# Performance work log

Measured on AMD Instinct MI355X. Metric: run time of the kernel, lower is better.

## Reference

```python
import jax, jax.numpy as jnp
import numpy as np

B, C, N = 8, 3, 4096
NSAMPLE = 10
MLP = (64, 64)
# checkerboard re-gather pattern from the original module
INDS = np.array([0, 1, 2, 3, 2, 3, 4, 5, 4, 5, 6, 7, 6, 7, 8, 9])


def setup_inputs() -> dict:
    key = jax.random.key(0)
    k1, k2, k3 = jax.random.split(key, 3)
    pos = jax.random.normal(k1, (B, C, N), jnp.float32)
    w1 = jax.random.normal(k2, (MLP[0], 4 * C, 2, 2), jnp.float32) * 0.1  # Conv2d(12, mlp0, k=2)
    b1 = jnp.zeros((MLP[0],), jnp.float32)
    w2 = jax.random.normal(k3, (MLP[1], MLP[0]), jnp.float32) * 0.1       # Conv2d(mlp0, mlp1, k=1)
    b2 = jnp.zeros((MLP[1],), jnp.float32)
    return {"pos": pos, "w1": w1, "b1": b1, "w2": w2, "b2": b2}


def _squeeze_2x2_alt(x):
    # x: [B, N, c, 4, 4] -> [B, N, 4c, 2, 2] with channel order [a, d, b, c]
    a = x[..., 0::2, 0::2]  # (0,0) of each 2x2 block
    d = x[..., 1::2, 1::2]  # (1,1)
    b = x[..., 0::2, 1::2]  # (0,1)
    c = x[..., 1::2, 0::2]  # (1,0)
    return jnp.concatenate([a, d, b, c], axis=-3)


def reference(pos, w1, b1, w2, b2):
    Bn, Cn, Nn = pos.shape
    pos_t = pos.transpose(0, 2, 1)  # [B, N, C]
    # pairwise squared distances [B, N, N]
    sq = jnp.sum(pos_t * pos_t, axis=-1)
    d2 = sq[:, :, None] - 2.0 * jnp.einsum('bnc,bmc->bnm', pos_t, pos_t) + sq[:, None, :]
    _, idx = jax.lax.top_k(-d2, NSAMPLE)  # [B, N, K] nearest neighbors (self first)
    # grouping_operation: grouped[b,c,n,k] = pos[b,c,idx[b,n,k]]
    grouped = jax.vmap(lambda p, i: p[:, i])(pos, idx)  # [B, C, N, K]
    pg = grouped[..., INDS]                              # [B, C, N, 16]
    pg = pg.transpose(0, 2, 1, 3).reshape(Bn, Nn, Cn, 4, 4)  # [B, N, 3, 4, 4]
    sqz = _squeeze_2x2_alt(pg)                           # [B, N, 12, 2, 2]
    # Conv2d(12->mlp0, k=2, stride=1) over 2x2 spatial == full contraction
    h = jnp.einsum('bnchw,ochw->bno', sqz, w1) + b1      # [B, N, mlp0]
    out = jnp.einsum('bno,po->bnp', h, w2) + b2          # [B, N, mlp1]
    return out.transpose(0, 2, 1)                        # [B, mlp1, N]
```

## Files before the change

kernel.cpp:

```cpp
#include <hip/hip_runtime.h>
#include <math.h>

#define NPTS 4096
#define NSMP 10

typedef float f32x2 __attribute__((ext_vector_type(2)));

__global__ __launch_bounds__(256) void prep_kernel(
    const float* __restrict__ w1, const float* __restrict__ b1,
    const float* __restrict__ w2, const float* __restrict__ b2,
    float* __restrict__ wn, float* __restrict__ bb) {
  __shared__ float w1l[64 * 48];
  __shared__ float w2t[64 * 64];
  __shared__ float b1l[64];
  __shared__ float part[4][30][64];
  __shared__ float bpart[4][64];
  const int t = threadIdx.x, p = t & 63, grp = t >> 6, o0 = grp * 16;
  for (int idx = t; idx < 64 * 48; idx += 256) w1l[idx] = w1[idx];
  for (int idx = t; idx < 64 * 64; idx += 256) w2t[(idx & 63) * 64 + (idx >> 6)] = w2[idx];
  if (t < 64) b1l[t] = b1[t];
  __syncthreads();

  const int sg[16] = {0,2,4,6, 3,5,7,9, 1,3,5,7, 2,4,6,8};
  float w2r[16];
  #pragma unroll
  for (int oo = 0; oo < 16; ++oo) w2r[oo] = w2t[(o0 + oo) * 64 + p];
  float wloc[30];
  #pragma unroll
  for (int i = 0; i < 30; ++i) wloc[i] = 0.0f;
  #pragma unroll
  for (int g = 0; g < 4; ++g)
    #pragma unroll
    for (int i = 0; i < 2; ++i)
      #pragma unroll
      for (int j = 0; j < 2; ++j) {
        const int s = sg[g * 4 + i * 2 + j];
        #pragma unroll
        for (int c = 0; c < 3; ++c) {
          const int k = (c + 3 * g) * 4 + i * 2 + j;
          float wk = 0.0f;
          #pragma unroll
          for (int oo = 0; oo < 16; ++oo)
            wk = fmaf(w2r[oo], w1l[(o0 + oo) * 48 + k], wk);
          wloc[s * 3 + c] += wk;
        }
      }
  #pragma unroll
  for (int i = 0; i < 30; ++i) part[grp][i][p] = wloc[i];
  float sb = 0.0f;
  #pragma unroll
  for (int oo = 0; oo < 16; ++oo) sb = fmaf(w2r[oo], b1l[o0 + oo], sb);
  bpart[grp][p] = sb;
  __syncthreads();
  const float* p0 = &part[0][0][0];
  for (int idx = t; idx < 30 * 64; idx += 256)
    wn[idx] = p0[idx] + p0[1920 + idx] + p0[3840 + idx] + p0[5760 + idx];
  if (t < 64) bb[t] = b2[t] + bpart[0][t] + bpart[1][t] + bpart[2][t] + bpart[3][t];
}

__global__ __launch_bounds__(1024, 4) void topk_kernel(const float* __restrict__ pos,
                                                       const float* __restrict__ wng,
                                                       const float* __restrict__ bbg,
                                                       float* __restrict__ out) {
  __shared__ float4 pts[NPTS];
  __shared__ int cnt[16][8];
  __shared__ int bufi[16][8][64];
  __shared__ int nbrL[16][8][NSMP];

  const int b = blockIdx.y, tid = threadIdx.x, lane = tid & 63, wv = tid >> 6;
  const float* pb = pos + (size_t)b * 3 * NPTS;
  for (int i = tid; i < NPTS; i += 1024) {
    float x = pb[i], y = pb[i + NPTS], z = pb[i + 2 * NPTS];
    float sq = __fadd_rn(__fadd_rn(__fmul_rn(x, x), __fmul_rn(y, y)), __fmul_rn(z, z));
    pts[i] = make_float4(x, y, z, sq);
  }
  float wnr[30];
  #pragma unroll
  for (int sc = 0; sc < 30; ++sc) wnr[sc] = wng[sc * 64 + lane];
  const float blv = bbg[lane];
  __syncthreads();

  const int n0 = blockIdx.x * 128 + wv * 8;

  f32x2 qx2[4], qy2[4], qz2[4], dmin[4];
  #pragma unroll
  for (int pp = 0; pp < 4; ++pp) {
    float4 qa = pts[n0 + 2 * pp], qb = pts[n0 + 2 * pp + 1];
    qx2[pp].x = -2.0f * qa.x; qx2[pp].y = -2.0f * qb.x;
    qy2[pp].x = -2.0f * qa.y; qy2[pp].y = -2.0f * qb.y;
    qz2[pp].x = -2.0f * qa.z; qz2[pp].y = -2.0f * qb.z;
    dmin[pp].x = INFINITY; dmin[pp].y = INFINITY;
  }

  #pragma unroll 8
  for (int k = 0; k < 64; ++k) {
    float4 p = pts[k * 64 + lane];
    #pragma unroll
    for (int pp = 0; pp < 4; ++pp) {
      f32x2 key = qx2[pp] * p.x + p.w;
      key = qy2[pp] * p.y + key;
      key = qz2[pp] * p.z + key;
      dmin[pp] = __builtin_elementwise_min(dmin[pp], key);
    }
  }

  unsigned um[8], lo[8], hi[8];
  #pragma unroll
  for (int r = 0; r < 8; ++r) {
    float dm = (r & 1) ? dmin[r >> 1].y : dmin[r >> 1].x;
    unsigned ub = __float_as_uint(dm);
    um[r] = (ub & 0x80000000u) ? ~ub : (ub | 0x80000000u);
    lo[r] = 0u; hi[r] = 0xFFFFFFFFu;
  }
  #pragma unroll 1
  for (int it = 0; it < 20; ++it) {
    #pragma unroll
    for (int r = 0; r < 8; ++r) {
      unsigned mid = lo[r] + ((hi[r] - lo[r]) >> 1);
      int c10 = __popcll(__ballot(um[r] <= mid));
      if (c10 >= NSMP) hi[r] = mid; else lo[r] = mid + 1;
    }
  }
  float tx[8];
  #pragma unroll
  for (int r = 0; r < 8; ++r) {
    unsigned tb = (hi[r] & 0x80000000u) ? (hi[r] ^ 0x80000000u) : ~hi[r];
    float tf = __uint_as_float(tb);
    tx[r] = __fadd_rn(__fadd_rn(tf, 2e-4f), __fmul_rn(fabsf(tf), 1e-5f));
  }

  if (lane < 8) cnt[wv][lane] = 0;

  #pragma unroll 4
  for (int k = 0; k < 64; ++k) {
    float4 p = pts[k * 64 + lane];
    #pragma unroll
    for (int pp = 0; pp < 4; ++pp) {
      f32x2 key = qx2[pp] * p.x + p.w;
      key = qy2[pp] * p.y + key;
      key = qz2[pp] * p.z + key;
      if (key.x <= tx[2 * pp]) {
        int ps = atomicAdd(&cnt[wv][2 * pp], 1);
        if (ps < 64) bufi[wv][2 * pp][ps] = k * 64 + lane;
      }
      if (key.y <= tx[2 * pp + 1]) {
        int ps = atomicAdd(&cnt[wv][2 * pp + 1], 1);
        if (ps < 64) bufi[wv][2 * pp + 1][ps] = k * 64 + lane;
      }
    }
  }

  int c[8], si[8], rank[8];
  double dd[8];
  int cmax = 0;
  #pragma unroll
  for (int r = 0; r < 8; ++r) {
    c[r] = __builtin_amdgcn_readfirstlane(cnt[wv][r]);
    if (c[r] > 64) c[r] = 64;
    cmax = (c[r] > cmax) ? c[r] : cmax;
    rank[r] = 0;
  }
  #pragma unroll
  for (int r = 0; r < 8; ++r) {
    float4 qa = pts[n0 + r];
    if (lane < c[r]) {
      si[r] = bufi[wv][r][lane];
      float4 p = pts[si[r]];
      double dqx = (double)qa.x, dqy = (double)qa.y, dqz = (double)qa.z;
      double px = (double)p.x, py = (double)p.y, pz = (double)p.z;
      double dot = dqx * px + dqy * py + dqz * pz;
      double sqn = dqx * dqx + dqy * dqy + dqz * dqz;
      double sqm = px * px + py * py + pz * pz;
      dd[r] = (sqn - 2.0 * dot) + sqm;
    } else { dd[r] = (double)INFINITY; si[r] = 0x7FFFFFFF; }
  }
  #pragma unroll 1
  for (int j = 0; j < cmax; ++j) {
    #pragma unroll
    for (int r = 0; r < 8; ++r) {
      int jlo = __builtin_amdgcn_readlane(__double2loint(dd[r]), j);
      int jhi = __builtin_amdgcn_readlane(__double2hiint(dd[r]), j);
      int ji  = __builtin_amdgcn_readlane(si[r], j);
      double jd = __hiloint2double(jhi, jlo);
      if (jd < dd[r] || (jd == dd[r] && ji < si[r])) ++rank[r];
    }
  }
  #pragma unroll
  for (int r = 0; r < 8; ++r)
    if (lane < c[r] && rank[r] < NSMP)
      nbrL[wv][r][rank[r]] = si[r];

  float acc[8];
  #pragma unroll
  for (int r = 0; r < 8; ++r) acc[r] = blv;
  #pragma unroll 1
  for (int r = 0; r < 8; ++r) {
    float a = acc[r];
    #pragma unroll
    for (int s = 0; s < NSMP; ++s) {
      int id = nbrL[wv][r][s];
      float4 pv = pts[id];
      a = fmaf(wnr[s * 3 + 0], pv.x, a);
      a = fmaf(wnr[s * 3 + 1], pv.y, a);
      a = fmaf(wnr[s * 3 + 2], pv.z, a);
    }
    acc[r] = a;
  }
  float* ob = out + ((size_t)b * 64 + lane) * NPTS + n0;
  float4 v0 = make_float4(acc[0], acc[1], acc[2], acc[3]);
  float4 v1 = make_float4(acc[4], acc[5], acc[6], acc[7]);
  *(float4*)(ob)     = v0;
  *(float4*)(ob + 4) = v1;
}

extern "C" void kernel_launch(void* const* d_in, const int* in_sizes, int n_in,
                              void* d_out, int out_size, void* d_ws, size_t ws_size,
                              hipStream_t stream) {
  (void)in_sizes; (void)n_in; (void)out_size; (void)ws_size;
  const float* pos = (const float*)d_in[0];
  const float* w1  = (const float*)d_in[1];
  const float* b1  = (const float*)d_in[2];
  const float* w2  = (const float*)d_in[3];
  const float* b2  = (const float*)d_in[4];
  float* out = (float*)d_out;

  float* wn = (float*)d_ws;
  float* bb = (float*)((char*)d_ws + 30 * 64 * 4);

  prep_kernel<<<dim3(1), dim3(256), 0, stream>>>(w1, b1, w2, b2, wn, bb);
  topk_kernel<<<dim3(32, 8), dim3(1024), 0, stream>>>(pos, wn, bb, out);
}
```

Before: 135.7 us.

## Fuse weight folding into top-k kernel, radix-select threshold, coalesced LDS-staged output

Removes the separate single-block prep kernel and instead has every block fold w2·w1 (and the bias) into shared memory after staging a transposed w2, which saves one launch and its serialization. The binary-search threshold is replaced with a bitwise radix prefix search that runs 24 ballot rounds instead of 20 with simpler arithmetic. Output is staged through shared memory, reusing the candidate buffer region, and written as coalesced float4 rows instead of strided per-lane 8-float stores. Each of the 256 blocks now redundantly recomputes the folded weights and reads them from LDS in the final MLP step instead of registers. The squared norm also changes to fma form.

```diff
diff --git a/kernel.cpp b/kernel.cpp
--- a/kernel.cpp
+++ b/kernel.cpp
@@ -6,81 +6,65 @@
 
 typedef float f32x2 __attribute__((ext_vector_type(2)));
 
-__global__ __launch_bounds__(256) void prep_kernel(
-    const float* __restrict__ w1, const float* __restrict__ b1,
-    const float* __restrict__ w2, const float* __restrict__ b2,
-    float* __restrict__ wn, float* __restrict__ bb) {
-  __shared__ float w1l[64 * 48];
-  __shared__ float w2t[64 * 64];
-  __shared__ float b1l[64];
-  __shared__ float part[4][30][64];
-  __shared__ float bpart[4][64];
-  const int t = threadIdx.x, p = t & 63, grp = t >> 6, o0 = grp * 16;
-  for (int idx = t; idx < 64 * 48; idx += 256) w1l[idx] = w1[idx];
-  for (int idx = t; idx < 64 * 64; idx += 256) w2t[(idx & 63) * 64 + (idx >> 6)] = w2[idx];
-  if (t < 64) b1l[t] = b1[t];
-  __syncthreads();
-
-  const int sg[16] = {0,2,4,6, 3,5,7,9, 1,3,5,7, 2,4,6,8};
-  float w2r[16];
-  #pragma unroll
-  for (int oo = 0; oo < 16; ++oo) w2r[oo] = w2t[(o0 + oo) * 64 + p];
-  float wloc[30];
-  #pragma unroll
-  for (int i = 0; i < 30; ++i) wloc[i] = 0.0f;
-  #pragma unroll
-  for (int g = 0; g < 4; ++g)
-    #pragma unroll
-    for (int i = 0; i < 2; ++i)
-      #pragma unroll
-      for (int j = 0; j < 2; ++j) {
-        const int s = sg[g * 4 + i * 2 + j];
-        #pragma unroll
-        for (int c = 0; c < 3; ++c) {
-          const int k = (c + 3 * g) * 4 + i * 2 + j;
-          float wk = 0.0f;
-          #pragma unroll
-          for (int oo = 0; oo < 16; ++oo)
-            wk = fmaf(w2r[oo], w1l[(o0 + oo) * 48 + k], wk);
-          wloc[s * 3 + c] += wk;
-        }
-      }
-  #pragma unroll
-  for (int i = 0; i < 30; ++i) part[grp][i][p] = wloc[i];
-  float sb = 0.0f;
-  #pragma unroll
-  for (int oo = 0; oo < 16; ++oo) sb = fmaf(w2r[oo], b1l[o0 + oo], sb);
-  bpart[grp][p] = sb;
-  __syncthreads();
-  const float* p0 = &part[0][0][0];
-  for (int idx = t; idx < 30 * 64; idx += 256)
-    wn[idx] = p0[idx] + p0[1920 + idx] + p0[3840 + idx] + p0[5760 + idx];
-  if (t < 64) bb[t] = b2[t] + bpart[0][t] + bpart[1][t] + bpart[2][t] + bpart[3][t];
-}
-
 __global__ __launch_bounds__(1024, 4) void topk_kernel(const float* __restrict__ pos,
-                                                       const float* __restrict__ wng,
-                                                       const float* __restrict__ bbg,
+                                                       const float* __restrict__ w1,
+                                                       const float* __restrict__ b1,
+                                                       const float* __restrict__ w2,
+                                                       const float* __restrict__ b2,
                                                        float* __restrict__ out) {
   __shared__ float4 pts[NPTS];
-  __shared__ int cnt[16][8];
-  __shared__ int bufi[16][8][64];
-  __shared__ int nbrL[16][8][NSMP];
+  __shared__ float  trans[16 * 520];
+  __shared__ float  wl[30 * 64];
+  __shared__ float  bl[64];
+  __shared__ int    nbrL[16][8][NSMP];
+  __shared__ int    cnt[16][8];
 
   const int b = blockIdx.y, tid = threadIdx.x, lane = tid & 63, wv = tid >> 6;
   const float* pb = pos + (size_t)b * 3 * NPTS;
   for (int i = tid; i < NPTS; i += 1024) {
     float x = pb[i], y = pb[i + NPTS], z = pb[i + 2 * NPTS];
-    float sq = __fadd_rn(__fadd_rn(__fmul_rn(x, x), __fmul_rn(y, y)), __fmul_rn(z, z));
+    float sq = fmaf(z, z, fmaf(y, y, x * x));
     pts[i] = make_float4(x, y, z, sq);
   }
-  float wnr[30];
-  #pragma unroll
-  for (int sc = 0; sc < 30; ++sc) wnr[sc] = wng[sc * 64 + lane];
-  const float blv = bbg[lane];
+  for (int idx = tid; idx < 4096; idx += 1024)
+    trans[(idx & 63) * 65 + (idx >> 6)] = w2[idx];
   __syncthreads();
 
-  const int n0 = blockIdx.x * 128 + wv * 8;
+  {
+    const int occN[10] = {1,1,2,2,2,2,2,2,1,1};
+    const int occG[10][2] = {{0,0},{2,0},{0,3},{1,2},{0,3},{1,2},{0,3},{1,2},{3,0},{1,0}};
+    const int occQ[10][2] = {{0,0},{0,0},{1,0},{0,1},{2,1},{1,2},{3,2},{2,3},{3,0},{3,0}};
+    if (wv < 15) {
+      #pragma unroll
+      for (int slot = 0; slot < 2; ++slot) {
+        int sc = wv + 15 * slot;
+        int s = sc / 3, cc = sc - 3 * s;
+        int k1 = __builtin_amdgcn_readfirstlane((cc + 3 * occG[s][0]) * 4 + occQ[s][0]);
+        int k2 = __builtin_amdgcn_readfirstlane((cc + 3 * occG[s][1]) * 4 + occQ[s][1]);
+        int two = __builtin_amdgcn_readfirstlane(occN[s] - 1);
+        float acc = 0.0f;
+        #pragma unroll 8
+        for (int o = 0; o < 64; ++o) {
+          float wsum = w1[o * 48 + k1];
+          if (two) wsum += w1[o * 48 + k2];
+          acc = fmaf(trans[o * 65 + lane], wsum, acc);
+        }
+        wl[sc * 64 + lane] = acc;
+      }
+    } else {
+      float acc = b2[lane];
+      #pragma unroll 8
+      for (int o = 0; o < 64; ++o)
+        acc = fmaf(trans[o * 65 + lane], b1[o], acc);
+      bl[lane] = acc;
+    }
+  }
+  __syncthreads();
+
+  const int nb = blockIdx.x * 128;
+  const int n0 = nb + wv * 8;
+  float* transF = &trans[wv * 520];
+  int*   bufiW  = (int*)transF;
 
   f32x2 qx2[4], qy2[4], qz2[4], dmin[4];
   #pragma unroll
@@ -104,27 +88,26 @@
     }
   }
 
-  unsigned um[8], lo[8], hi[8];
+  unsigned um[8];
   #pragma unroll
   for (int r = 0; r < 8; ++r) {
     float dm = (r & 1) ? dmin[r >> 1].y : dmin[r >> 1].x;
     unsigned ub = __float_as_uint(dm);
     um[r] = (ub & 0x80000000u) ? ~ub : (ub | 0x80000000u);
-    lo[r] = 0u; hi[r] = 0xFFFFFFFFu;
-  }
+  }
+  unsigned pfx[8] = {0u,0u,0u,0u,0u,0u,0u,0u};
   #pragma unroll 1
-  for (int it = 0; it < 20; ++it) {
-    #pragma unroll
-    for (int r = 0; r < 8; ++r) {
-      unsigned mid = lo[r] + ((hi[r] - lo[r]) >> 1);
-      int c10 = __popcll(__ballot(um[r] <= mid));
-      if (c10 >= NSMP) hi[r] = mid; else lo[r] = mid + 1;
-    }
+  for (int bno = 31; bno >= 8; --bno) {
+    const unsigned bit = 1u << bno, ones = bit - 1u;
+    #pragma unroll
+    for (int r = 0; r < 8; ++r)
+      if (__popcll(__ballot(um[r] <= (pfx[r] | ones))) < NSMP) pfx[r] |= bit;
   }
   float tx[8];
   #pragma unroll
   for (int r = 0; r < 8; ++r) {
-    unsigned tb = (hi[r] & 0x80000000u) ? (hi[r] ^ 0x80000000u) : ~hi[r];
+    unsigned T = pfx[r] | 0xFFu;
+    unsigned tb = (T & 0x80000000u) ? (T ^ 0x80000000u) : ~T;
     float tf = __uint_as_float(tb);
     tx[r] = __fadd_rn(__fadd_rn(tf, 2e-4f), __fmul_rn(fabsf(tf), 1e-5f));
   }
@@ -141,11 +124,11 @@
       key = qz2[pp] * p.z + key;
       if (key.x <= tx[2 * pp]) {
         int ps = atomicAdd(&cnt[wv][2 * pp], 1);
-        if (ps < 64) bufi[wv][2 * pp][ps] = k * 64 + lane;
+        if (ps < 64) bufiW[(2 * pp) * 64 + ps] = k * 64 + lane;
       }
       if (key.y <= tx[2 * pp + 1]) {
         int ps = atomicAdd(&cnt[wv][2 * pp + 1], 1);
-        if (ps < 64) bufi[wv][2 * pp + 1][ps] = k * 64 + lane;
+        if (ps < 64) bufiW[(2 * pp + 1) * 64 + ps] = k * 64 + lane;
       }
     }
   }
@@ -164,13 +147,13 @@
   for (int r = 0; r < 8; ++r) {
     float4 qa = pts[n0 + r];
     if (lane < c[r]) {
-      si[r] = bufi[wv][r][lane];
+      si[r] = bufiW[r * 64 + lane];
       float4 p = pts[si[r]];
       double dqx = (double)qa.x, dqy = (double)qa.y, dqz = (double)qa.z;
-      double px = (double)p.x, py = (double)p.y, pz = (double)p.z;
-      double dot = dqx * px + dqy * py + dqz * pz;
+      double dpx = (double)p.x, dpy = (double)p.y, dpz = (double)p.z;
+      double dot = dqx * dpx + dqy * dpy + dqz * dpz;
       double sqn = dqx * dqx + dqy * dqy + dqz * dqz;
-      double sqm = px * px + py * py + pz * pz;
+      double sqm = dpx * dpx + dpy * dpy + dpz * dpz;
       dd[r] = (sqn - 2.0 * dot) + sqm;
     } else { dd[r] = (double)INFINITY; si[r] = 0x7FFFFFFF; }
   }
@@ -190,33 +173,35 @@
     if (lane < c[r] && rank[r] < NSMP)
       nbrL[wv][r][rank[r]] = si[r];
 
-  float acc[8];
-  #pragma unroll
-  for (int r = 0; r < 8; ++r) acc[r] = blv;
   #pragma unroll 1
   for (int r = 0; r < 8; ++r) {
-    float a = acc[r];
+    float a = bl[lane];
     #pragma unroll
     for (int s = 0; s < NSMP; ++s) {
       int id = nbrL[wv][r][s];
       float4 pv = pts[id];
-      a = fmaf(wnr[s * 3 + 0], pv.x, a);
-      a = fmaf(wnr[s * 3 + 1], pv.y, a);
-      a = fmaf(wnr[s * 3 + 2], pv.z, a);
-    }
-    acc[r] = a;
-  }
-  float* ob = out + ((size_t)b * 64 + lane) * NPTS + n0;
-  float4 v0 = make_float4(acc[0], acc[1], acc[2], acc[3]);
-  float4 v1 = make_float4(acc[4], acc[5], acc[6], acc[7]);
-  *(float4*)(ob)     = v0;
-  *(float4*)(ob + 4) = v1;
+      a = fmaf(wl[(s * 3 + 0) * 64 + lane], pv.x, a);
+      a = fmaf(wl[(s * 3 + 1) * 64 + lane], pv.y, a);
+      a = fmaf(wl[(s * 3 + 2) * 64 + lane], pv.z, a);
+    }
+    transF[r * 65 + lane] = a;
+  }
+  __syncthreads();
+
+  #pragma unroll
+  for (int it = 0; it < 2; ++it) {
+    int p = (tid >> 5) + 32 * it, t32 = tid & 31;
+    const float* src = &trans[(t32 >> 1) * 520 + (t32 & 1) * 4 * 65 + p];
+    float4 v;
+    v.x = src[0 * 65]; v.y = src[1 * 65]; v.z = src[2 * 65]; v.w = src[3 * 65];
+    *(float4*)(out + ((size_t)b * 64 + p) * NPTS + nb + 4 * t32) = v;
+  }
 }
 
 extern "C" void kernel_launch(void* const* d_in, const int* in_sizes, int n_in,
                               void* d_out, int out_size, void* d_ws, size_t ws_size,
                               hipStream_t stream) {
-  (void)in_sizes; (void)n_in; (void)out_size; (void)ws_size;
+  (void)in_sizes; (void)n_in; (void)out_size; (void)d_ws; (void)ws_size;
   const float* pos = (const float*)d_in[0];
   const float* w1  = (const float*)d_in[1];
   const float* b1  = (const float*)d_in[2];
@@ -224,9 +209,5 @@
   const float* b2  = (const float*)d_in[4];
   float* out = (float*)d_out;
 
-  float* wn = (float*)d_ws;
-  float* bb = (float*)((char*)d_ws + 30 * 64 * 4);
-
-  prep_kernel<<<dim3(1), dim3(256), 0, stream>>>(w1, b1, w2, b2, wn, bb);
-  topk_kernel<<<dim3(32, 8), dim3(1024), 0, stream>>>(pos, wn, bb, out);
+  topk_kernel<<<dim3(32, 8), dim3(1024), 0, stream>>>(pos, w1, b1, w2, b2, out);
 }
```

Measured after the change: 141.2 us. 4.1% more time.
